# Kernel tuning notes

Hardware: AMD Instinct MI355X
Metric: run time of the kernel (lower is better)

Reference implementation:

```python
import jax, jax.numpy as jnp
import numpy as np

B, C, H, W = 8, 192, 128, 128
HEADS = 16
EPS = 1e-12  # F.normalize eps


def setup_inputs() -> dict:
    key = jax.random.key(0)
    k1, k2, k3, k4 = jax.random.split(key, 4)
    s = 0.02
    return {
        "x": jax.random.normal(k1, (B, C, H, W), dtype=jnp.float32),
        "w_qkv": jax.random.normal(k2, (3 * C, C), dtype=jnp.float32) * s,
        "w_dw": jax.random.normal(k3, (C, 1, 3, 3), dtype=jnp.float32) * s,
        "w_proj": jax.random.normal(k4, (C, C), dtype=jnp.float32) * s,
        "temperature": jnp.ones((HEADS, 1, 1), dtype=jnp.float32),
    }


def reference(x, w_qkv, w_dw, w_proj, temperature):
    b, c, h, w = x.shape
    heads = HEADS
    hd = c // heads  # per-head channel dim
    hw = h * w

    # 1x1 conv qkv projection: [b, 3c, h, w]
    qkv = jnp.einsum('bchw,oc->bohw', x, w_qkv)
    q, k, v = jnp.split(qkv, 3, axis=1)

    def to_heads(t):
        return t.reshape(b, heads, hd, hw)  # b head c (h w)

    q, k, v = to_heads(q), to_heads(k), to_heads(v)

    # L2-normalize along spatial dim (matches F.normalize with eps clamp)
    q = q / jnp.maximum(jnp.linalg.norm(q, axis=-1, keepdims=True), EPS)
    k = k / jnp.maximum(jnp.linalg.norm(k, axis=-1, keepdims=True), EPS)

    # channel-wise attention: [b, head, hd, hd]
    attn = jnp.einsum('bhcn,bhdn->bhcd', q, k) * temperature
    attn = jax.nn.softmax(attn, axis=-1)

    out = jnp.einsum('bhcd,bhdn->bhcn', attn, v)  # [b, head, hd, hw]
    out = out.reshape(b, c, h, w)

    # depthwise 3x3 conv, padding=1
    out = jax.lax.conv_general_dilated(
        out, w_dw, window_strides=(1, 1), padding=((1, 1), (1, 1)),
        dimension_numbers=('NCHW', 'OIHW', 'NCHW'), feature_group_count=c)

    # 1x1 conv projection
    out = jnp.einsum('bchw,oc->bohw', out, w_proj)
    return out
```

## Files before the change

kernel.cpp:

```cpp
#include <hip/hip_runtime.h>

#define B_   8
#define C_   192
#define HW_  16384
#define W_   128
#define NH_  16
#define HD_  12

#define OFF_G      0u
#define OFF_WQKV   1179648u
#define OFF_WDW    1622016u
#define OFF_TEMP   1628928u
#define OFF_WPROJ  1629184u
#define OFF_M      1702912u
#define OFF_Y      2292736u

typedef __attribute__((ext_vector_type(8))) __bf16 bf16x8;
typedef __attribute__((ext_vector_type(8))) short  short8;
typedef __attribute__((ext_vector_type(4))) short  short4v;
typedef __attribute__((ext_vector_type(4))) float  floatx4;

__device__ __forceinline__ unsigned short f2bfu(float f) {
  union { float f; unsigned u; } v; v.f = f;
  unsigned r = (v.u + 0x7FFFu + ((v.u >> 16) & 1u)) >> 16;
  return (unsigned short)r;
}
__device__ __forceinline__ float bfu2f(unsigned short h) {
  union { unsigned u; float f; } v; v.u = ((unsigned)h) << 16;
  return v.f;
}
__device__ __forceinline__ bool bfmode(const void* temp) {
  return ((const unsigned*)temp)[0] != 0x3F800000u;
}
__device__ __forceinline__ float in_ld(const void* p, int i, bool bf) {
  return bf ? bfu2f(((const unsigned short*)p)[i]) : ((const float*)p)[i];
}
__device__ __forceinline__ floatx4 mfma16(short8 a, short8 b, floatx4 c) {
  union U { short8 s; bf16x8 b; } ua, ub;
  ua.s = a; ub.s = b;
  return __builtin_amdgcn_mfma_f32_16x16x32_bf16(ua.b, ub.b, c, 0, 0, 0);
}
__device__ __forceinline__ short8 row_frag(const void* x, bool bf, long elemoff) {
  short8 r;
  if (bf) {
    r = *(const short8*)((const unsigned short*)x + elemoff);
  } else {
    const float4* p4 = (const float4*)((const float*)x + elemoff);
    float4 a = p4[0], b = p4[1];
    r[0] = (short)f2bfu(a.x); r[1] = (short)f2bfu(a.y);
    r[2] = (short)f2bfu(a.z); r[3] = (short)f2bfu(a.w);
    r[4] = (short)f2bfu(b.x); r[5] = (short)f2bfu(b.y);
    r[6] = (short)f2bfu(b.z); r[7] = (short)f2bfu(b.w);
  }
  return r;
}

__global__ __launch_bounds__(256) void k_init(const void* wqkv, const void* wdw,
                                              const void* wproj, const void* temp,
                                              unsigned char* ws) {
  bool bf = bfmode(temp);
  int idx = blockIdx.x * 256 + threadIdx.x;
  if (idx < 294912) { ((float*)(ws + OFF_G))[idx] = 0.f; return; }
  int i = idx - 294912;
  if (i < 110592) { ((float*)(ws + OFF_WQKV))[i] = in_ld(wqkv, i, bf); return; }
  i -= 110592;
  if (i < 1728) { ((float*)(ws + OFF_WDW))[i] = in_ld(wdw, i, bf); return; }
  i -= 1728;
  if (i < 16) { ((float*)(ws + OFF_TEMP))[i] = in_ld(temp, i, bf); return; }
  i -= 16;
  if (i < 36864) {
    unsigned short* wp = (unsigned short*)(ws + OFF_WPROJ);
    wp[i] = bf ? ((const unsigned short*)wproj)[i] : f2bfu(((const float*)wproj)[i]);
  }
}

__global__ __launch_bounds__(256) void k_gram(const void* x, const void* temp,
                                              unsigned char* ws) {
  bool bf = bfmode(temp);
  float* G = (float*)(ws + OFF_G);
  int b = blockIdx.x >> 6, grp = blockIdx.x & 63;
  int tid = threadIdx.x;
  int w = tid >> 6, lane = tid & 63, m = lane & 15, q = lane >> 4;
  long xb = (long)b * C_ * HW_;
  __shared__ __align__(16) short xs[C_][136];
  floatx4 acc[3][12];
  floatx4 zz = {0.f, 0.f, 0.f, 0.f};
  for (int i = 0; i < 3; ++i)
    for (int t = 0; t < 12; ++t) acc[i][t] = zz;
  for (int sl = 0; sl < 2; ++sl) {
    int px0 = (grp * 2 + sl) * 128;
    if (sl) __syncthreads();
    for (int i = 0; i < 12; ++i) {
      int chunk = i * 256 + tid;
      int c = chunk >> 4, p8 = chunk & 15;
      short8 v = row_frag(x, bf, xb + (long)c * HW_ + px0 + p8 * 8);
      *(short8*)&xs[c][p8 * 8] = v;
    }
    __syncthreads();
    for (int ks = 0; ks < 4; ++ks) {
      int col = ks * 32 + q * 8;
      short8 A0 = *(const short8*)&xs[(3 * w + 0) * 16 + m][col];
      short8 A1 = *(const short8*)&xs[(3 * w + 1) * 16 + m][col];
      short8 A2 = *(const short8*)&xs[(3 * w + 2) * 16 + m][col];
      for (int t = 0; t < 12; ++t) {
        short8 F = *(const short8*)&xs[t * 16 + m][col];
        acc[0][t] = mfma16(A0, F, acc[0][t]);
        acc[1][t] = mfma16(A1, F, acc[1][t]);
        acc[2][t] = mfma16(A2, F, acc[2][t]);
      }
    }
  }
  for (int i = 0; i < 3; ++i)
    for (int t = 0; t < 12; ++t)
      for (int r = 0; r < 4; ++r)
        atomicAdd(&G[((long)b * C_ + (3 * w + i) * 16 + q * 4 + r) * C_ + t * 16 + m],
                  acc[i][t][r]);
}

__global__ __launch_bounds__(256) void k_attn(unsigned char* ws) {
  int b = blockIdx.x >> 4, h = blockIdx.x & 15;
  int tid = threadIdx.x;
  const float* G  = (const float*)(ws + OFF_G) + (long)b * C_ * C_;
  const float* Wf = (const float*)(ws + OFF_WQKV);
  const float* Wq = Wf + (h * HD_) * C_;
  const float* Wk = Wf + (C_ + h * HD_) * C_;
  const float* Wv = Wf + (2 * C_ + h * HD_) * C_;
  float tmprt = ((const float*)(ws + OFF_TEMP))[h];
  unsigned short* Mh = (unsigned short*)(ws + OFF_M) + ((long)b * C_ + h * HD_) * C_;

  __shared__ float Gs[32][C_ + 1];
  __shared__ float tq[HD_][C_], tk[HD_][C_];
  __shared__ float Sm[HD_][HD_], Aw[HD_][HD_], nq[HD_], nk[HD_];

  for (int jblk = 0; jblk < 6; ++jblk) {
    for (int i = tid; i < 32 * C_; i += 256) {
      int jj = i / C_, a = i - jj * C_;
      Gs[jj][a] = G[(jblk * 32 + jj) * C_ + a];
    }
    __syncthreads();
    for (int i = tid; i < 2 * HD_ * 32; i += 256) {
      int jj = i & 31, rest = i >> 5;
      int c = rest % HD_, which = rest / HD_;
      const float* Wrow = (which ? Wk : Wq) + c * C_;
      float s = 0.f;
      for (int a = 0; a < C_; ++a) s += Wrow[a] * Gs[jj][a];
      float (*dst)[C_] = which ? tk : tq;
      dst[c][jblk * 32 + jj] = s;
    }
    __syncthreads();
  }
  if (tid < 144) {
    int c = tid / HD_, d = tid - c * HD_;
    float s = 0.f;
    for (int a = 0; a < C_; ++a) s += tq[c][a] * Wk[d * C_ + a];
    Sm[c][d] = s;
  } else if (tid < 156) {
    int c = tid - 144; float s = 0.f;
    for (int a = 0; a < C_; ++a) s += tq[c][a] * Wq[c * C_ + a];
    nq[c] = s;
  } else if (tid < 168) {
    int c = tid - 156; float s = 0.f;
    for (int a = 0; a < C_; ++a) s += tk[c][a] * Wk[c * C_ + a];
    nk[c] = s;
  }
  __syncthreads();
  if (tid < HD_) {
    int c = tid;
    float qn = fmaxf(sqrtf(fmaxf(nq[c], 0.f)), 1e-12f);
    float L[HD_], mx = -1e30f;
    for (int d = 0; d < HD_; ++d) {
      float kn = fmaxf(sqrtf(fmaxf(nk[d], 0.f)), 1e-12f);
      L[d] = Sm[c][d] / (qn * kn) * tmprt;
      mx = fmaxf(mx, L[d]);
    }
    float ssum = 0.f;
    for (int d = 0; d < HD_; ++d) { L[d] = __expf(L[d] - mx); ssum += L[d]; }
    float inv = 1.f / ssum;
    for (int d = 0; d < HD_; ++d) Aw[c][d] = L[d] * inv;
  }
  __syncthreads();
  for (int i = tid; i < HD_ * C_; i += 256) {
    int c = i / C_, j = i - c * C_;
    float s = 0.f;
    for (int d = 0; d < HD_; ++d) s += Aw[c][d] * Wv[d * C_ + j];
    Mh[c * C_ + j] = f2bfu(s);
  }
}

__global__ __launch_bounds__(256) void k_mx(const void* x, const void* temp,
                                            unsigned char* ws) {
  bool bf = bfmode(temp);
  const unsigned short* Mb = (const unsigned short*)(ws + OFF_M);
  unsigned short* y = (unsigned short*)(ws + OFF_Y);
  int b = blockIdx.x >> 7, px0 = (blockIdx.x & 127) * 128;
  int tid = threadIdx.x;
  int w = tid >> 6, lane = tid & 63, m = lane & 15, q = lane >> 4;
  long xb = (long)b * C_ * HW_;
  __shared__ __align__(16) short xsT[128][200];
  for (int i = 0; i < 3; ++i) {
    int chunk = i * 256 + tid;
    int p8 = chunk & 15, cq = chunk >> 4;
    short8 r0 = row_frag(x, bf, xb + (long)(cq * 4 + 0) * HW_ + px0 + p8 * 8);
    short8 r1 = row_frag(x, bf, xb + (long)(cq * 4 + 1) * HW_ + px0 + p8 * 8);
    short8 r2 = row_frag(x, bf, xb + (long)(cq * 4 + 2) * HW_ + px0 + p8 * 8);
    short8 r3 = row_frag(x, bf, xb + (long)(cq * 4 + 3) * HW_ + px0 + p8 * 8);
    for (int j = 0; j < 8; ++j) {
      short4v v = { r0[j], r1[j], r2[j], r3[j] };
      *(short4v*)&xsT[p8 * 8 + j][cq * 4] = v;
    }
  }
  __syncthreads();
  floatx4 acc[3][8];
  floatx4 zz = {0.f, 0.f, 0.f, 0.f};
  for (int i = 0; i < 3; ++i)
    for (int pt = 0; pt < 8; ++pt) acc[i][pt] = zz;
  for (int k = 0; k < 6; ++k) {
    int c0 = k * 32;
    const unsigned short* Mrow = Mb + (long)b * C_ * C_ + c0 + q * 8;
    short8 A0 = *(const short8*)(Mrow + ((3 * w + 0) * 16 + m) * C_);
    short8 A1 = *(const short8*)(Mrow + ((3 * w + 1) * 16 + m) * C_);
    short8 A2 = *(const short8*)(Mrow + ((3 * w + 2) * 16 + m) * C_);
    for (int pt = 0; pt < 8; ++pt) {
      short8 Bf = *(const short8*)&xsT[pt * 16 + m][c0 + q * 8];
      acc[0][pt] = mfma16(A0, Bf, acc[0][pt]);
      acc[1][pt] = mfma16(A1, Bf, acc[1][pt]);
      acc[2][pt] = mfma16(A2, Bf, acc[2][pt]);
    }
  }
  for (int i = 0; i < 3; ++i) {
    int rowb = (3 * w + i) * 16 + q * 4;
    for (int pt = 0; pt < 8; ++pt) {
      int px = px0 + pt * 16 + m;
      for (int rg = 0; rg < 4; ++rg)
        y[((long)b * C_ + rowb + rg) * HW_ + px] = f2bfu(acc[i][pt][rg]);
    }
  }
}

__global__ __launch_bounds__(512) void k_out(const void* temp, unsigned char* ws,
                                             void* out) {
  bool bf = bfmode(temp);
  const unsigned short* y = (const unsigned short*)(ws + OFF_Y);
  const float* wdw = (const float*)(ws + OFF_WDW);
  const unsigned short* Wp = (const unsigned short*)(ws + OFF_WPROJ);
  int b = blockIdx.x >> 7, irow = blockIdx.x & 127;
  int tid = threadIdx.x;
  __shared__ __align__(16) unsigned dly[128 * 36];

  int wv = tid >> 6, lane = tid & 63, m = lane & 15, q = lane >> 4;
  int wr = wv >> 2, wc = wv & 3;
  int pA = wc * 32 + m, pB = pA + 16;
  int swzA = (pA >> 3) & 7, swzB = (pB >> 3) & 7;

  int oct = tid & 15, cg = tid >> 4;
  int p0 = oct * 8;
  int wbase = p0 * 36 + ((((cg >> 2) ^ (oct & 7)) << 2) | (cg & 3));

  floatx4 acc[6][2];
  floatx4 zz = {0.f, 0.f, 0.f, 0.f};
#pragma unroll
  for (int r = 0; r < 6; ++r) { acc[r][0] = zz; acc[r][1] = zz; }

  for (int ch = 0; ch < 3; ++ch) {
    if (ch) __syncthreads();
    float a0[8], a1[8];
#pragma unroll
    for (int i = 0; i < 8; ++i) { a0[i] = 0.f; a1[i] = 0.f; }
#pragma unroll
    for (int j = 0; j < 2; ++j) {
      float* aj = j ? a1 : a0;
      int c = ch * 64 + cg * 2 + j;
      const unsigned short* yc = y + ((long)b * C_ + c) * HW_;
      float wv9[9];
#pragma unroll
      for (int t = 0; t < 9; ++t) wv9[t] = wdw[c * 9 + t];
      for (int dy = 0; dy < 3; ++dy) {
        int rr = irow + dy - 1;
        if (rr < 0 || rr > 127) continue;
        const unsigned short* yr = yc + rr * W_;
        float v[10];
        v[0] = (p0 == 0) ? 0.f : bfu2f(yr[p0 - 1]);
        union { uint4 u; unsigned short s[8]; } uu;
        uu.u = *(const uint4*)(yr + p0);
#pragma unroll
        for (int i = 0; i < 8; ++i) v[1 + i] = bfu2f(uu.s[i]);
        v[9] = (p0 + 8 >= W_) ? 0.f : bfu2f(yr[p0 + 8]);
#pragma unroll
        for (int dx = 0; dx < 3; ++dx) {
          float wc9 = wv9[dy * 3 + dx];
#pragma unroll
          for (int i = 0; i < 8; ++i) aj[i] += wc9 * v[i + dx];
        }
      }
    }
#pragma unroll
    for (int i = 0; i < 8; ++i) {
      unsigned pk = (unsigned)f2bfu(a0[i]) | ((unsigned)f2bfu(a1[i]) << 16);
      dly[wbase + i * 36] = pk;
    }
    __syncthreads();
#pragma unroll
    for (int ks = 0; ks < 2; ++ks) {
      int kb = ks * 4 + q;
      short8 B0 = *(const short8*)&dly[pA * 36 + ((kb ^ swzA) << 2)];
      short8 B1 = *(const short8*)&dly[pB * 36 + ((kb ^ swzB) << 2)];
      int c0 = ch * 64 + ks * 32 + q * 8;
#pragma unroll
      for (int r = 0; r < 6; ++r) {
        short8 A = *(const short8*)(Wp + (wr * 96 + r * 16 + m) * C_ + c0);
        acc[r][0] = mfma16(A, B0, acc[r][0]);
        acc[r][1] = mfma16(A, B1, acc[r][1]);
      }
    }
  }
  long ob = (long)b * C_ * HW_ + irow * W_;
#pragma unroll
  for (int r = 0; r < 6; ++r) {
    int o = wr * 96 + r * 16 + q * 4;
#pragma unroll
    for (int rg = 0; rg < 4; ++rg) {
      long off = ob + (long)(o + rg) * HW_;
      float v0 = acc[r][0][rg], v1 = acc[r][1][rg];
      if (bf) {
        ((unsigned short*)out)[off + pA] = f2bfu(v0);
        ((unsigned short*)out)[off + pB] = f2bfu(v1);
      } else {
        ((float*)out)[off + pA] = v0;
        ((float*)out)[off + pB] = v1;
      }
    }
  }
}

extern "C" void kernel_launch(void* const* d_in, const int* in_sizes, int n_in,
                              void* d_out, int out_size, void* d_ws, size_t ws_size,
                              hipStream_t stream) {
  const void* x     = d_in[0];
  const void* wqkv  = d_in[1];
  const void* wdw   = d_in[2];
  const void* wproj = d_in[3];
  const void* temp  = d_in[4];
  unsigned char* ws = (unsigned char*)d_ws;
  k_init<<<dim3(1735), dim3(256), 0, stream>>>(wqkv, wdw, wproj, temp, ws);
  k_gram<<<dim3(512), dim3(256), 0, stream>>>(x, temp, ws);
  k_attn<<<dim3(128), dim3(256), 0, stream>>>(ws);
  k_mx<<<dim3(1024), dim3(256), 0, stream>>>(x, temp, ws);
  k_out<<<dim3(1024), dim3(512), 0, stream>>>(temp, ws, d_out);
}
```

Before: 399.5 us.

## Replace Gram atomics with partial buffers, register-prefetch x slices, 512-thread blocks

The Gram kernel now runs 256 blocks of 512 threads, each covering 512 pixels over four 128-pixel slices. The next slice is prefetched into registers while the current one is consumed by MFMA, so global loads overlap compute. Instead of atomically adding into G, each block writes its partial 192x192 Gram to a scratch region, and a new reduce kernel sums the 32 partials per batch. This removes the zero-init of G and the atomic contention, at the cost of an extra launch and about 38 MB of partial writes and reads.

```diff
diff --git a/kernel.cpp b/kernel.cpp
--- a/kernel.cpp
+++ b/kernel.cpp
@@ -59,9 +59,7 @@
                                               const void* wproj, const void* temp,
                                               unsigned char* ws) {
   bool bf = bfmode(temp);
-  int idx = blockIdx.x * 256 + threadIdx.x;
-  if (idx < 294912) { ((float*)(ws + OFF_G))[idx] = 0.f; return; }
-  int i = idx - 294912;
+  int i = blockIdx.x * 256 + threadIdx.x;
   if (i < 110592) { ((float*)(ws + OFF_WQKV))[i] = in_ld(wqkv, i, bf); return; }
   i -= 110592;
   if (i < 1728) { ((float*)(ws + OFF_WDW))[i] = in_ld(wdw, i, bf); return; }
@@ -74,47 +72,90 @@
   }
 }
 
-__global__ __launch_bounds__(256) void k_gram(const void* x, const void* temp,
+__global__ __launch_bounds__(512) void k_gram(const void* x, const void* temp,
                                               unsigned char* ws) {
   bool bf = bfmode(temp);
-  float* G = (float*)(ws + OFF_G);
-  int b = blockIdx.x >> 6, grp = blockIdx.x & 63;
+  float* GP = (float*)(ws + OFF_Y);
+  int b = blockIdx.x >> 5, grp = blockIdx.x & 31;
   int tid = threadIdx.x;
   int w = tid >> 6, lane = tid & 63, m = lane & 15, q = lane >> 4;
+  int r0 = (w >> 1) * 3, c0 = (w & 1) * 6;
   long xb = (long)b * C_ * HW_;
   __shared__ __align__(16) short xs[C_][136];
-  floatx4 acc[3][12];
+  floatx4 acc[3][6];
   floatx4 zz = {0.f, 0.f, 0.f, 0.f};
+#pragma unroll
   for (int i = 0; i < 3; ++i)
-    for (int t = 0; t < 12; ++t) acc[i][t] = zz;
-  for (int sl = 0; sl < 2; ++sl) {
-    int px0 = (grp * 2 + sl) * 128;
+#pragma unroll
+    for (int t = 0; t < 6; ++t) acc[i][t] = zz;
+
+  short8 st[6];
+  {
+    int px0 = grp * 512;
+#pragma unroll
+    for (int i = 0; i < 6; ++i) {
+      int chunk = i * 512 + tid;
+      int c = chunk >> 4, p8 = chunk & 15;
+      st[i] = row_frag(x, bf, xb + (long)c * HW_ + px0 + p8 * 8);
+    }
+  }
+  for (int sl = 0; sl < 4; ++sl) {
     if (sl) __syncthreads();
-    for (int i = 0; i < 12; ++i) {
-      int chunk = i * 256 + tid;
+#pragma unroll
+    for (int i = 0; i < 6; ++i) {
+      int chunk = i * 512 + tid;
       int c = chunk >> 4, p8 = chunk & 15;
-      short8 v = row_frag(x, bf, xb + (long)c * HW_ + px0 + p8 * 8);
-      *(short8*)&xs[c][p8 * 8] = v;
+      *(short8*)&xs[c][p8 * 8] = st[i];
     }
     __syncthreads();
+    if (sl < 3) {
+      int px0 = grp * 512 + (sl + 1) * 128;
+#pragma unroll
+      for (int i = 0; i < 6; ++i) {
+        int chunk = i * 512 + tid;
+        int c = chunk >> 4, p8 = chunk & 15;
+        st[i] = row_frag(x, bf, xb + (long)c * HW_ + px0 + p8 * 8);
+      }
+    }
+#pragma unroll
     for (int ks = 0; ks < 4; ++ks) {
       int col = ks * 32 + q * 8;
-      short8 A0 = *(const short8*)&xs[(3 * w + 0) * 16 + m][col];
-      short8 A1 = *(const short8*)&xs[(3 * w + 1) * 16 + m][col];
-      short8 A2 = *(const short8*)&xs[(3 * w + 2) * 16 + m][col];
-      for (int t = 0; t < 12; ++t) {
-        short8 F = *(const short8*)&xs[t * 16 + m][col];
+      short8 A0 = *(const short8*)&xs[(r0 + 0) * 16 + m][col];
+      short8 A1 = *(const short8*)&xs[(r0 + 1) * 16 + m][col];
+      short8 A2 = *(const short8*)&xs[(r0 + 2) * 16 + m][col];
+#pragma unroll
+      for (int t = 0; t < 6; ++t) {
+        short8 F = *(const short8*)&xs[(c0 + t) * 16 + m][col];
         acc[0][t] = mfma16(A0, F, acc[0][t]);
         acc[1][t] = mfma16(A1, F, acc[1][t]);
         acc[2][t] = mfma16(A2, F, acc[2][t]);
       }
     }
   }
+  float* GPb = GP + (long)(b * 32 + grp) * (C_ * C_);
+#pragma unroll
   for (int i = 0; i < 3; ++i)
-    for (int t = 0; t < 12; ++t)
+#pragma unroll
+    for (int t = 0; t < 6; ++t)
+#pragma unroll
       for (int r = 0; r < 4; ++r)
-        atomicAdd(&G[((long)b * C_ + (3 * w + i) * 16 + q * 4 + r) * C_ + t * 16 + m],
-                  acc[i][t][r]);
+        GPb[((r0 + i) * 16 + q * 4 + r) * C_ + (c0 + t) * 16 + m] = acc[i][t][r];
+}
+
+__global__ __launch_bounds__(256) void k_reduce(unsigned char* ws) {
+  const float4* GP = (const float4*)(ws + OFF_Y);
+  float4* G = (float4*)(ws + OFF_G);
+  int idx = blockIdx.x * 256 + threadIdx.x;
+  int b = idx / 9216;
+  int i = idx - b * 9216;
+  const float4* p = GP + (long)b * 32 * 9216 + i;
+  float4 s = {0.f, 0.f, 0.f, 0.f};
+#pragma unroll
+  for (int g = 0; g < 32; ++g) {
+    float4 v = p[(long)g * 9216];
+    s.x += v.x; s.y += v.y; s.z += v.z; s.w += v.w;
+  }
+  G[(long)b * 9216 + i] = s;
 }
 
 __global__ __launch_bounds__(256) void k_attn(unsigned char* ws) {
@@ -341,8 +382,9 @@
   const void* wproj = d_in[3];
   const void* temp  = d_in[4];
   unsigned char* ws = (unsigned char*)d_ws;
-  k_init<<<dim3(1735), dim3(256), 0, stream>>>(wqkv, wdw, wproj, temp, ws);
-  k_gram<<<dim3(512), dim3(256), 0, stream>>>(x, temp, ws);
+  k_init<<<dim3(583), dim3(256), 0, stream>>>(wqkv, wdw, wproj, temp, ws);
+  k_gram<<<dim3(256), dim3(512), 0, stream>>>(x, temp, ws);
+  k_reduce<<<dim3(288), dim3(256), 0, stream>>>(ws);
   k_attn<<<dim3(128), dim3(256), 0, stream>>>(ws);
   k_mx<<<dim3(1024), dim3(256), 0, stream>>>(x, temp, ws);
   k_out<<<dim3(1024), dim3(512), 0, stream>>>(temp, ws, d_out);
```

Measured after the change: 349.1 us. 12.6% less time.
